# Kernel optimization log

Hardware: AMD Instinct MI355X
Metric: run time of the kernel (lower is better)

Reference implementation:

```python
import jax, jax.numpy as jnp
import numpy as np

N, L, D, H = 2, 2048, 2048, 16
HD = D // H  # head_dim = 128


def setup_inputs() -> dict:
    key = jax.random.key(0)
    k1, k2, k3, k4 = jax.random.split(key, 4)
    x = jax.random.normal(k1, (N, L, D), dtype=jnp.float32)
    pos = jax.random.normal(k2, (2, L, HD), dtype=jnp.float32)
    w_qkv = jax.random.normal(k3, (3 * D, D), dtype=jnp.float32) * (D ** -0.5)
    w_o = jax.random.normal(k4, (D, D), dtype=jnp.float32) * (D ** -0.5)
    return {"x": x, "pos": pos, "w_qkv": w_qkv, "w_o": w_o}


def rotate_half(t):
    t1, t2 = jnp.split(t, 2, axis=-1)
    return jnp.concatenate((-t2, t1), axis=-1)


def reference(x, pos, w_qkv, w_o):
    n, l, d = x.shape
    h, hd = H, HD
    qkv = jnp.einsum('nld,ed->nle', x, w_qkv)  # [N,L,3D]
    q, k, v = jnp.split(qkv, 3, axis=-1)
    q = q.reshape(n, l, h, hd)
    k = k.reshape(n, l, h, hd)
    v = v.reshape(n, l, h, hd)
    cos = pos[0][None, :, None, :]  # [1,L,1,HD]
    sin = pos[1][None, :, None, :]
    q = q * cos + rotate_half(q) * sin
    k = k * cos + rotate_half(k) * sin
    scale = hd ** -0.5
    scores = jnp.einsum('nlhd,nmhd->nhlm', q, k) * scale  # [N,H,L,L]
    causal = jnp.tril(jnp.ones((l, l), dtype=bool))
    scores = jnp.where(causal[None, None], scores, jnp.finfo(scores.dtype).min)
    attn = jax.nn.softmax(scores, axis=-1)
    o = jnp.einsum('nhlm,nmhd->nlhd', attn, v).reshape(n, l, d)
    return jnp.einsum('nld,ed->nle', o, w_o)
```

## Files before the change

### kernel.cpp

```cpp
#include <hip/hip_runtime.h>
#include <hip/hip_bf16.h>

typedef __attribute__((ext_vector_type(8))) short short8;
typedef __attribute__((ext_vector_type(4))) float f32x4;
typedef __attribute__((ext_vector_type(2))) unsigned uint2v;

#define NB 2
#define SEQ 2048
#define DM 2048
#define NHEAD 16
#define HDIM 128

__device__ __forceinline__ unsigned short f2bf(float f) {
    unsigned u = __float_as_uint(f);
    u += 0x7fffu + ((u >> 16) & 1u);
    return (unsigned short)(u >> 16);
}
__device__ __forceinline__ float bf2f(unsigned short h) {
    return __uint_as_float(((unsigned)h) << 16);
}
__device__ __forceinline__ unsigned pk2bf(float a, float b) {
    __hip_bfloat162 h = __float22bfloat162_rn(make_float2(a, b));
    return *reinterpret_cast<unsigned*>(&h);
}
__device__ __forceinline__ void gload16(const unsigned short* g, unsigned short* l) {
    __builtin_amdgcn_global_load_lds((const __attribute__((address_space(1))) void*)g,
                                     (__attribute__((address_space(3))) void*)l,
                                     16, 0, 0);
}

__global__ __launch_bounds__(256) void cvt_bf16(const float* __restrict__ a,
                                                unsigned short* __restrict__ oa, int na8,
                                                const float* __restrict__ b,
                                                unsigned short* __restrict__ ob, int nb8)
{
    const int t0 = blockIdx.x * 256 + threadIdx.x;
    const int stride = gridDim.x * 256;
    for (int i = t0; i < na8; i += stride) {
        const f32x4* src = (const f32x4*)(a + (size_t)i * 8);
        f32x4 lo = src[0], hi = src[1];
        short8 v;
#pragma unroll
        for (int j = 0; j < 4; ++j) { v[j] = (short)f2bf(lo[j]); v[j + 4] = (short)f2bf(hi[j]); }
        *(short8*)(oa + (size_t)i * 8) = v;
    }
    for (int i = t0; i < nb8; i += stride) {
        const f32x4* src = (const f32x4*)(b + (size_t)i * 8);
        f32x4 lo = src[0], hi = src[1];
        short8 v;
#pragma unroll
        for (int j = 0; j < 4; ++j) { v[j] = (short)f2bf(lo[j]); v[j + 4] = (short)f2bf(hi[j]); }
        *(short8*)(ob + (size_t)i * 8) = v;
    }
}

template<int EPI, int CPX>
__global__ __launch_bounds__(256) void gemm_m97(const unsigned short* __restrict__ A,
                                                const unsigned short* __restrict__ B,
                                                int K,
                                                unsigned short* __restrict__ qb,
                                                unsigned short* __restrict__ kb,
                                                unsigned short* __restrict__ vtb,
                                                const float* __restrict__ posp,
                                                float* __restrict__ outf)
{
    __shared__ unsigned short smem[16384];
    const int tid = threadIdx.x;
    const int lane = tid & 63, w = tid >> 6;
    const int wr = w >> 1, wc = w & 1;
    const int g = lane >> 4, fr = lane & 15;
    const int lr = lane >> 2, ls = lane & 3;
    const int x = blockIdx.x & 7, t = blockIdx.x >> 3;
    const int rp = t / (2 * CPX), wi = t % (2 * CPX);
    const int bx = x * CPX + (wi % CPX), by = rp * 2 + wi / CPX;
    const int row0 = by * 128, col0 = bx * 128;

    auto stage = [&](int b, int kt) {
        const int k0 = kt * 32;
#pragma unroll
        for (int c = 0; c < 2; ++c) {
            const int r = c * 64 + w * 16;
            gload16(A + (size_t)(row0 + r + lr) * K + k0 + ls * 8,
                    smem + b * 4096 + r * 32);
            gload16(B + (size_t)(col0 + r + lr) * K + k0 + ls * 8,
                    smem + 8192 + b * 4096 + r * 32);
        }
    };

    const f32x4 fz = {0.f, 0.f, 0.f, 0.f};
    f32x4 acc[4][4];
#pragma unroll
    for (int m = 0; m < 4; ++m)
#pragma unroll
        for (int n = 0; n < 4; ++n) acc[m][n] = fz;

    const int nk = K / 32;
    stage(0, 0);
    __syncthreads();
    for (int kt = 0; kt < nk; ++kt) {
        const int cur = kt & 1;
        if (kt + 1 < nk) stage(cur ^ 1, kt + 1);
        short8 af[4], bfv[4];
#pragma unroll
        for (int m = 0; m < 4; ++m)
            af[m] = *(const short8*)&smem[cur * 4096 + (wr * 64 + m * 16 + fr) * 32 + g * 8];
#pragma unroll
        for (int n = 0; n < 4; ++n)
            bfv[n] = *(const short8*)&smem[8192 + cur * 4096 + (wc * 64 + n * 16 + fr) * 32 + g * 8];
#pragma unroll
        for (int m = 0; m < 4; ++m)
#pragma unroll
            for (int n = 0; n < 4; ++n)
                acc[m][n] = __builtin_amdgcn_mfma_f32_16x16x32_bf16(
                    af[m], bfv[n], acc[m][n], 0, 0, 0);
        __syncthreads();
    }

    if constexpr (EPI == 0) {
#pragma unroll
        for (int m = 0; m < 4; ++m)
#pragma unroll
            for (int n = 0; n < 4; ++n)
#pragma unroll
                for (int r = 0; r < 4; ++r) {
                    int rr = row0 + wr * 64 + m * 16 + g * 4 + r;
                    int cc = col0 + wc * 64 + n * 16 + fr;
                    outf[(size_t)rr * 2048 + cc] = acc[m][n][r];
                }
    } else {
        const int which = col0 >> 11;
        const int hB = (col0 >> 7) & 15;
        const int nb_ = row0 >> 11;
        const size_t hb = (size_t)(nb_ * NHEAD + hB) * ((size_t)SEQ * HDIM);
        const int l0 = row0 & 2047;
        if (which < 2) {
#pragma unroll
            for (int m = 0; m < 4; ++m)
#pragma unroll
                for (int n = 0; n < 4; ++n)
#pragma unroll
                    for (int r = 0; r < 4; ++r) {
                        int rl = wr * 64 + m * 16 + g * 4 + r;
                        int cl = wc * 64 + n * 16 + fr;
                        smem[rl * 128 + (cl ^ ((rl & 7) * 8))] = f2bf(acc[m][n][r]);
                    }
            __syncthreads();
            unsigned short* dst = which ? kb : qb;
            const int rg = tid >> 4;
            const int s8 = (tid & 15) * 8;
            const float sgn = (s8 < 64) ? -1.f : 1.f;
#pragma unroll
            for (int j = 0; j < 8; ++j) {
                int rl = j * 16 + rg;
                int l = l0 + rl;
                int sw = (rl & 7) * 8;
                short8 own = *(const short8*)&smem[rl * 128 + (s8 ^ sw)];
                short8 par = *(const short8*)&smem[rl * 128 + ((s8 ^ 64) ^ sw)];
                const float* cp = posp + (size_t)l * HDIM + s8;
                const float* sp = cp + (size_t)SEQ * HDIM;
                f32x4 c0 = *(const f32x4*)cp, c1 = *(const f32x4*)(cp + 4);
                f32x4 s0 = *(const f32x4*)sp, s1 = *(const f32x4*)(sp + 4);
                short8 res;
#pragma unroll
                for (int e = 0; e < 8; ++e) {
                    float cc = (e < 4) ? c0[e & 3] : c1[e & 3];
                    float ss = (e < 4) ? s0[e & 3] : s1[e & 3];
                    float o = bf2f((unsigned short)own[e]);
                    float p = bf2f((unsigned short)par[e]);
                    res[e] = (short)f2bf(o * cc + sgn * p * ss);
                }
                *(short8*)(dst + hb + (size_t)l * HDIM + s8) = res;
            }
        } else {
#pragma unroll
            for (int m = 0; m < 4; ++m)
#pragma unroll
                for (int n = 0; n < 4; ++n) {
                    int lb = l0 + wr * 64 + m * 16 + g * 4;
                    int cl = wc * 64 + n * 16 + fr;
                    uint2v v;
                    v[0] = pk2bf(acc[m][n][0], acc[m][n][1]);
                    v[1] = pk2bf(acc[m][n][2], acc[m][n][3]);
                    *(uint2v*)(vtb + hb + (size_t)cl * SEQ + lb) = v;
                }
        }
    }
}

__global__ __launch_bounds__(256, 2) void attn_k(const unsigned short* __restrict__ Q,
                                                 const unsigned short* __restrict__ K,
                                                 const unsigned short* __restrict__ VT,
                                                 unsigned short* __restrict__ O)
{
    const int lb = blockIdx.x;
    const int half = lb >> 8;
    const int r0 = lb & 255;
    const int xcd = r0 & 7, idx = r0 >> 3;
    const int nh = xcd * 4 + (idx & 3);
    const int j = idx >> 2;
    const int tile = half ? j : (15 - j);
    const int tid = threadIdx.x;
    const int w = tid >> 6, lane = tid & 63;
    const int g = lane >> 4, fr = lane & 15;
    const float scale = 0.08838834764831845f;

    const unsigned short* Qh = Q + (size_t)nh * SEQ * HDIM;
    const unsigned short* Kh = K + (size_t)nh * SEQ * HDIM;
    const unsigned short* Vh = VT + (size_t)nh * SEQ * HDIM;
    const int nb = nh >> 4, h = nh & 15;

    __shared__ unsigned short Kt[2][8192];
    __shared__ unsigned short Vt[2][8192];
    __shared__ unsigned Plds[4][576];

    auto stage = [&](int bf, int kbi) {
        const int key0 = kbi * 64;
#pragma unroll
        for (int c = 0; c < 4; ++c) {
            int r = c * 16 + (tid >> 4);
            int sK = tid & 15;
            gload16(Kh + (size_t)(key0 + r) * HDIM + 8 * (sK ^ (r & 7)),
                    &Kt[bf][c * 2048 + w * 512]);
            int d = c * 32 + (tid >> 3);
            int sV = tid & 7;
            gload16(Vh + (size_t)d * SEQ + key0 + 8 * (sV ^ (d & 7)),
                    &Vt[bf][c * 2048 + w * 512]);
        }
    };

    const int qt = tile * 128 + w * 32;
    const int nkb_w = (qt + 31) >> 6;
    const int nkb_blk = 2 * tile + 1;

    short8 qf[2][4];
#pragma unroll
    for (int u = 0; u < 2; ++u)
#pragma unroll
        for (int kk = 0; kk < 4; ++kk)
            qf[u][kk] = *(const short8*)(Qh + (size_t)(qt + u * 16 + fr) * HDIM + kk * 32 + g * 8);

    const f32x4 fz = {0.f, 0.f, 0.f, 0.f};
    f32x4 oacc[2][8];
#pragma unroll
    for (int u = 0; u < 2; ++u)
#pragma unroll
        for (int f = 0; f < 8; ++f) oacc[u][f] = fz;
    float mrow[2] = {-3e38f, -3e38f}, lrow[2] = {0.f, 0.f};

    stage(0, 0);
    int buf = 0;
    __syncthreads();

    for (int kbi = 0; kbi <= nkb_blk; ++kbi) {
        if (kbi < nkb_blk) stage(buf ^ 1, kbi + 1);

        if (kbi <= nkb_w) {
            const int key0 = kbi * 64;
            f32x4 s[2][4];
#pragma unroll
            for (int u = 0; u < 2; ++u)
#pragma unroll
                for (int hh = 0; hh < 4; ++hh) s[u][hh] = fz;

            __builtin_amdgcn_s_setprio(1);
#pragma unroll
            for (int hh = 0; hh < 4; ++hh) {
                short8 kfh[4];
#pragma unroll
                for (int kk = 0; kk < 4; ++kk)
                    kfh[kk] = *(const short8*)&Kt[buf][(hh * 16 + fr) * 128 + 8 * ((4 * kk + g) ^ (fr & 7))];
#pragma unroll
                for (int u = 0; u < 2; ++u)
#pragma unroll
                    for (int kk = 0; kk < 4; ++kk)
                        s[u][hh] = __builtin_amdgcn_mfma_f32_16x16x32_bf16(kfh[kk], qf[u][kk], s[u][hh], 0, 0, 0);
            }
            __builtin_amdgcn_s_setprio(0);

#pragma unroll
            for (int u = 0; u < 2; ++u) {
                const int q = qt + u * 16 + fr;
#pragma unroll
                for (int hh = 0; hh < 4; ++hh)
#pragma unroll
                    for (int r = 0; r < 4; ++r) {
                        int key = key0 + hh * 16 + 4 * g + r;
                        float v = s[u][hh][r] * scale;
                        s[u][hh][r] = (key <= q) ? v : -1e30f;
                    }
                float mx = -3e38f;
#pragma unroll
                for (int hh = 0; hh < 4; ++hh)
                    mx = fmaxf(mx, fmaxf(fmaxf(s[u][hh][0], s[u][hh][1]),
                                         fmaxf(s[u][hh][2], s[u][hh][3])));
                mx = fmaxf(mx, __shfl_xor(mx, 16, 64));
                mx = fmaxf(mx, __shfl_xor(mx, 32, 64));
                if (!__all(mx <= mrow[u] + 8.f)) {
                    float mn = fmaxf(mrow[u], mx);
                    float al = __expf(mrow[u] - mn);
                    mrow[u] = mn;
                    lrow[u] *= al;
#pragma unroll
                    for (int f = 0; f < 8; ++f)
#pragma unroll
                        for (int r = 0; r < 4; ++r) oacc[u][f][r] *= al;
                }
                float pv[4][4];
                float ps = 0.f;
#pragma unroll
                for (int hh = 0; hh < 4; ++hh)
#pragma unroll
                    for (int r = 0; r < 4; ++r) {
                        float e = __expf(s[u][hh][r] - mrow[u]);
                        pv[hh][r] = e;
                        ps += e;
                    }
                ps += __shfl_xor(ps, 16, 64);
                ps += __shfl_xor(ps, 32, 64);
                lrow[u] += ps;
                unsigned* Pw = &Plds[w][0];
#pragma unroll
                for (int hh = 0; hh < 4; ++hh) {
                    Pw[fr * 36 + hh * 8 + 2 * g + 0] = pk2bf(pv[hh][0], pv[hh][1]);
                    Pw[fr * 36 + hh * 8 + 2 * g + 1] = pk2bf(pv[hh][2], pv[hh][3]);
                }
                asm volatile("s_waitcnt lgkmcnt(0)" ::: "memory");
                short8 pf0 = *(const short8*)&Pw[fr * 36 + g * 4];
                short8 pf1 = *(const short8*)&Pw[fr * 36 + 16 + g * 4];

                __builtin_amdgcn_s_setprio(1);
#pragma unroll
                for (int f = 0; f < 8; ++f) {
                    short8 vfa = *(const short8*)&Vt[buf][(f * 16 + fr) * 64 + 8 * (g ^ (fr & 7))];
                    short8 vfb = *(const short8*)&Vt[buf][(f * 16 + fr) * 64 + 8 * ((4 + g) ^ (fr & 7))];
                    oacc[u][f] = __builtin_amdgcn_mfma_f32_16x16x32_bf16(vfa, pf0, oacc[u][f], 0, 0, 0);
                    oacc[u][f] = __builtin_amdgcn_mfma_f32_16x16x32_bf16(vfb, pf1, oacc[u][f], 0, 0, 0);
                }
                __builtin_amdgcn_s_setprio(0);
            }
        }
        __syncthreads();
        buf ^= 1;
    }

#pragma unroll
    for (int u = 0; u < 2; ++u) {
        const float inv = 1.0f / lrow[u];
        const size_t obase = ((size_t)nb * SEQ + qt + u * 16 + fr) * DM + h * HDIM;
#pragma unroll
        for (int f = 0; f < 8; ++f) {
            uint2v v;
            v[0] = pk2bf(oacc[u][f][0] * inv, oacc[u][f][1] * inv);
            v[1] = pk2bf(oacc[u][f][2] * inv, oacc[u][f][3] * inv);
            *(uint2v*)(O + obase + f * 16 + 4 * g) = v;
        }
    }
}

extern "C" void kernel_launch(void* const* d_in, const int* in_sizes, int n_in,
                              void* d_out, int out_size, void* d_ws, size_t ws_size,
                              hipStream_t stream) {
    const float* x    = (const float*)d_in[0];
    const float* pos  = (const float*)d_in[1];
    const float* wqkv = (const float*)d_in[2];
    const float* wo   = (const float*)d_in[3];
    float* out = (float*)d_out;

    const size_t HBUF = (size_t)NB * NHEAD * SEQ * HDIM;
    unsigned short* qb   = (unsigned short*)d_ws;
    unsigned short* kbuf = qb + HBUF;
    unsigned short* vtb  = kbuf + HBUF;
    unsigned short* obx  = vtb + HBUF;
    unsigned short* wqkvbf = (unsigned short*)d_out;

    cvt_bf16<<<dim3(2048), 256, 0, stream>>>(x, obx, 1048576, wqkv, wqkvbf, 1572864);
    gemm_m97<1, 6><<<dim3(1536), 256, 0, stream>>>(obx, wqkvbf, 2048, qb, kbuf, vtb, pos, nullptr);
    attn_k<<<dim3(512), 256, 0, stream>>>(qb, kbuf, vtb, obx);
    cvt_bf16<<<dim3(512), 256, 0, stream>>>(wo, qb, 524288, wo, qb, 0);
    gemm_m97<0, 2><<<dim3(512), 256, 0, stream>>>(obx, qb, 2048, nullptr, nullptr, nullptr, nullptr, out);
}
```

Baseline: 282.1 us.

## Halve attention query tile to 64 rows and re-swizzle GEMM block order

```diff
diff --git a/kernel.cpp b/kernel.cpp
--- a/kernel.cpp
+++ b/kernel.cpp
@@ -54,7 +54,7 @@
     }
 }
 
-template<int EPI, int CPX>
+template<int EPI, int CPX, int CHALF>
 __global__ __launch_bounds__(256) void gemm_m97(const unsigned short* __restrict__ A,
                                                 const unsigned short* __restrict__ B,
                                                 int K,
@@ -70,9 +70,11 @@
     const int wr = w >> 1, wc = w & 1;
     const int g = lane >> 4, fr = lane & 15;
     const int lr = lane >> 2, ls = lane & 3;
+    constexpr int NSUB = CPX / CHALF;
     const int x = blockIdx.x & 7, t = blockIdx.x >> 3;
-    const int rp = t / (2 * CPX), wi = t % (2 * CPX);
-    const int bx = x * CPX + (wi % CPX), by = rp * 2 + wi / CPX;
+    const int ch = t / (32 * NSUB), u = t % (32 * NSUB);
+    const int rp = u / (2 * NSUB), wi = u % (2 * NSUB);
+    const int bx = x * CPX + ch * NSUB + (wi % NSUB), by = rp * 2 + wi / NSUB;
     const int row0 = by * 128, col0 = bx * 128;
 
     auto stage = [&](int b, int kt) {
@@ -193,12 +195,13 @@
                                                  unsigned short* __restrict__ O)
 {
     const int lb = blockIdx.x;
-    const int half = lb >> 8;
+    const int quart = lb >> 8;
     const int r0 = lb & 255;
     const int xcd = r0 & 7, idx = r0 >> 3;
     const int nh = xcd * 4 + (idx & 3);
     const int j = idx >> 2;
-    const int tile = half ? j : (15 - j);
+    const int tile = (quart == 0) ? (31 - j) : (quart == 1) ? j
+                   : (quart == 2) ? (23 - j) : (8 + j);
     const int tid = threadIdx.x;
     const int w = tid >> 6, lane = tid & 63;
     const int g = lane >> 4, fr = lane & 15;
@@ -228,132 +231,115 @@
         }
     };
 
-    const int qt = tile * 128 + w * 32;
-    const int nkb_w = (qt + 31) >> 6;
-    const int nkb_blk = 2 * tile + 1;
-
-    short8 qf[2][4];
-#pragma unroll
-    for (int u = 0; u < 2; ++u)
-#pragma unroll
-        for (int kk = 0; kk < 4; ++kk)
-            qf[u][kk] = *(const short8*)(Qh + (size_t)(qt + u * 16 + fr) * HDIM + kk * 32 + g * 8);
+    const int qt = tile * 64 + w * 16;
+    const int nkb = tile;
+
+    short8 qf[4];
+#pragma unroll
+    for (int kk = 0; kk < 4; ++kk)
+        qf[kk] = *(const short8*)(Qh + (size_t)(qt + fr) * HDIM + kk * 32 + g * 8);
 
     const f32x4 fz = {0.f, 0.f, 0.f, 0.f};
-    f32x4 oacc[2][8];
-#pragma unroll
-    for (int u = 0; u < 2; ++u)
-#pragma unroll
-        for (int f = 0; f < 8; ++f) oacc[u][f] = fz;
-    float mrow[2] = {-3e38f, -3e38f}, lrow[2] = {0.f, 0.f};
+    f32x4 oacc[8];
+#pragma unroll
+    for (int f = 0; f < 8; ++f) oacc[f] = fz;
+    float mrow = -3e38f, lrow = 0.f;
 
     stage(0, 0);
     int buf = 0;
     __syncthreads();
 
-    for (int kbi = 0; kbi <= nkb_blk; ++kbi) {
-        if (kbi < nkb_blk) stage(buf ^ 1, kbi + 1);
-
-        if (kbi <= nkb_w) {
-            const int key0 = kbi * 64;
-            f32x4 s[2][4];
-#pragma unroll
-            for (int u = 0; u < 2; ++u)
-#pragma unroll
-                for (int hh = 0; hh < 4; ++hh) s[u][hh] = fz;
-
-            __builtin_amdgcn_s_setprio(1);
-#pragma unroll
-            for (int hh = 0; hh < 4; ++hh) {
-                short8 kfh[4];
-#pragma unroll
-                for (int kk = 0; kk < 4; ++kk)
-                    kfh[kk] = *(const short8*)&Kt[buf][(hh * 16 + fr) * 128 + 8 * ((4 * kk + g) ^ (fr & 7))];
-#pragma unroll
-                for (int u = 0; u < 2; ++u)
-#pragma unroll
-                    for (int kk = 0; kk < 4; ++kk)
-                        s[u][hh] = __builtin_amdgcn_mfma_f32_16x16x32_bf16(kfh[kk], qf[u][kk], s[u][hh], 0, 0, 0);
+    for (int kbi = 0; kbi <= nkb; ++kbi) {
+        if (kbi < nkb) stage(buf ^ 1, kbi + 1);
+
+        const int key0 = kbi * 64;
+        f32x4 s[4];
+#pragma unroll
+        for (int hh = 0; hh < 4; ++hh) s[hh] = fz;
+
+        __builtin_amdgcn_s_setprio(1);
+#pragma unroll
+        for (int hh = 0; hh < 4; ++hh) {
+            short8 kfh[4];
+#pragma unroll
+            for (int kk = 0; kk < 4; ++kk)
+                kfh[kk] = *(const short8*)&Kt[buf][(hh * 16 + fr) * 128 + 8 * ((4 * kk + g) ^ (fr & 7))];
+#pragma unroll
+            for (int kk = 0; kk < 4; ++kk)
+                s[hh] = __builtin_amdgcn_mfma_f32_16x16x32_bf16(kfh[kk], qf[kk], s[hh], 0, 0, 0);
+        }
+        __builtin_amdgcn_s_setprio(0);
+
+        const int q = qt + fr;
+#pragma unroll
+        for (int hh = 0; hh < 4; ++hh)
+#pragma unroll
+            for (int r = 0; r < 4; ++r) {
+                int key = key0 + hh * 16 + 4 * g + r;
+                float v = s[hh][r] * scale;
+                s[hh][r] = (key <= q) ? v : -1e30f;
             }
-            __builtin_amdgcn_s_setprio(0);
-
-#pragma unroll
-            for (int u = 0; u < 2; ++u) {
-                const int q = qt + u * 16 + fr;
-#pragma unroll
-                for (int hh = 0; hh < 4; ++hh)
-#pragma unroll
-                    for (int r = 0; r < 4; ++r) {
-                        int key = key0 + hh * 16 + 4 * g + r;
-                        float v = s[u][hh][r] * scale;
-                        s[u][hh][r] = (key <= q) ? v : -1e30f;
-                    }
-                float mx = -3e38f;
-#pragma unroll
-                for (int hh = 0; hh < 4; ++hh)
-                    mx = fmaxf(mx, fmaxf(fmaxf(s[u][hh][0], s[u][hh][1]),
-                                         fmaxf(s[u][hh][2], s[u][hh][3])));
-                mx = fmaxf(mx, __shfl_xor(mx, 16, 64));
-                mx = fmaxf(mx, __shfl_xor(mx, 32, 64));
-                if (!__all(mx <= mrow[u] + 8.f)) {
-                    float mn = fmaxf(mrow[u], mx);
-                    float al = __expf(mrow[u] - mn);
-                    mrow[u] = mn;
-                    lrow[u] *= al;
-#pragma unroll
-                    for (int f = 0; f < 8; ++f)
-#pragma unroll
-                        for (int r = 0; r < 4; ++r) oacc[u][f][r] *= al;
-                }
-                float pv[4][4];
-                float ps = 0.f;
-#pragma unroll
-                for (int hh = 0; hh < 4; ++hh)
-#pragma unroll
-                    for (int r = 0; r < 4; ++r) {
-                        float e = __expf(s[u][hh][r] - mrow[u]);
-                        pv[hh][r] = e;
-                        ps += e;
-                    }
-                ps += __shfl_xor(ps, 16, 64);
-                ps += __shfl_xor(ps, 32, 64);
-                lrow[u] += ps;
-                unsigned* Pw = &Plds[w][0];
-#pragma unroll
-                for (int hh = 0; hh < 4; ++hh) {
-                    Pw[fr * 36 + hh * 8 + 2 * g + 0] = pk2bf(pv[hh][0], pv[hh][1]);
-                    Pw[fr * 36 + hh * 8 + 2 * g + 1] = pk2bf(pv[hh][2], pv[hh][3]);
-                }
-                asm volatile("s_waitcnt lgkmcnt(0)" ::: "memory");
-                short8 pf0 = *(const short8*)&Pw[fr * 36 + g * 4];
-                short8 pf1 = *(const short8*)&Pw[fr * 36 + 16 + g * 4];
-
-                __builtin_amdgcn_s_setprio(1);
-#pragma unroll
-                for (int f = 0; f < 8; ++f) {
-                    short8 vfa = *(const short8*)&Vt[buf][(f * 16 + fr) * 64 + 8 * (g ^ (fr & 7))];
-                    short8 vfb = *(const short8*)&Vt[buf][(f * 16 + fr) * 64 + 8 * ((4 + g) ^ (fr & 7))];
-                    oacc[u][f] = __builtin_amdgcn_mfma_f32_16x16x32_bf16(vfa, pf0, oacc[u][f], 0, 0, 0);
-                    oacc[u][f] = __builtin_amdgcn_mfma_f32_16x16x32_bf16(vfb, pf1, oacc[u][f], 0, 0, 0);
-                }
-                __builtin_amdgcn_s_setprio(0);
+        float mx = -3e38f;
+#pragma unroll
+        for (int hh = 0; hh < 4; ++hh)
+            mx = fmaxf(mx, fmaxf(fmaxf(s[hh][0], s[hh][1]), fmaxf(s[hh][2], s[hh][3])));
+        mx = fmaxf(mx, __shfl_xor(mx, 16, 64));
+        mx = fmaxf(mx, __shfl_xor(mx, 32, 64));
+        if (!__all(mx <= mrow + 8.f)) {
+            float mn = fmaxf(mrow, mx);
+            float al = __expf(mrow - mn);
+            mrow = mn;
+            lrow *= al;
+#pragma unroll
+            for (int f = 0; f < 8; ++f)
+#pragma unroll
+                for (int r = 0; r < 4; ++r) oacc[f][r] *= al;
+        }
+        float pv[4][4];
+        float ps = 0.f;
+#pragma unroll
+        for (int hh = 0; hh < 4; ++hh)
+#pragma unroll
+            for (int r = 0; r < 4; ++r) {
+                float e = __expf(s[hh][r] - mrow);
+                pv[hh][r] = e;
+                ps += e;
             }
-        }
+        ps += __shfl_xor(ps, 16, 64);
+        ps += __shfl_xor(ps, 32, 64);
+        lrow += ps;
+        unsigned* Pw = &Plds[w][0];
+#pragma unroll
+        for (int hh = 0; hh < 4; ++hh) {
+            Pw[fr * 36 + hh * 8 + 2 * g + 0] = pk2bf(pv[hh][0], pv[hh][1]);
+            Pw[fr * 36 + hh * 8 + 2 * g + 1] = pk2bf(pv[hh][2], pv[hh][3]);
+        }
+        asm volatile("s_waitcnt lgkmcnt(0)" ::: "memory");
+        short8 pf0 = *(const short8*)&Pw[fr * 36 + g * 4];
+        short8 pf1 = *(const short8*)&Pw[fr * 36 + 16 + g * 4];
+
+        __builtin_amdgcn_s_setprio(1);
+#pragma unroll
+        for (int f = 0; f < 8; ++f) {
+            short8 vfa = *(const short8*)&Vt[buf][(f * 16 + fr) * 64 + 8 * (g ^ (fr & 7))];
+            short8 vfb = *(const short8*)&Vt[buf][(f * 16 + fr) * 64 + 8 * ((4 + g) ^ (fr & 7))];
+            oacc[f] = __builtin_amdgcn_mfma_f32_16x16x32_bf16(vfa, pf0, oacc[f], 0, 0, 0);
+            oacc[f] = __builtin_amdgcn_mfma_f32_16x16x32_bf16(vfb, pf1, oacc[f], 0, 0, 0);
+        }
+        __builtin_amdgcn_s_setprio(0);
+
         __syncthreads();
         buf ^= 1;
     }
 
-#pragma unroll
-    for (int u = 0; u < 2; ++u) {
-        const float inv = 1.0f / lrow[u];
-        const size_t obase = ((size_t)nb * SEQ + qt + u * 16 + fr) * DM + h * HDIM;
-#pragma unroll
-        for (int f = 0; f < 8; ++f) {
-            uint2v v;
-            v[0] = pk2bf(oacc[u][f][0] * inv, oacc[u][f][1] * inv);
-            v[1] = pk2bf(oacc[u][f][2] * inv, oacc[u][f][3] * inv);
-            *(uint2v*)(O + obase + f * 16 + 4 * g) = v;
-        }
+    const float inv = 1.0f / lrow;
+    const size_t obase = ((size_t)nb * SEQ + qt + fr) * DM + h * HDIM;
+#pragma unroll
+    for (int f = 0; f < 8; ++f) {
+        uint2v v;
+        v[0] = pk2bf(oacc[f][0] * inv, oacc[f][1] * inv);
+        v[1] = pk2bf(oacc[f][2] * inv, oacc[f][3] * inv);
+        *(uint2v*)(O + obase + f * 16 + 4 * g) = v;
     }
 }
 
@@ -374,8 +360,8 @@
     unsigned short* wqkvbf = (unsigned short*)d_out;
 
     cvt_bf16<<<dim3(2048), 256, 0, stream>>>(x, obx, 1048576, wqkv, wqkvbf, 1572864);
-    gemm_m97<1, 6><<<dim3(1536), 256, 0, stream>>>(obx, wqkvbf, 2048, qb, kbuf, vtb, pos, nullptr);
-    attn_k<<<dim3(512), 256, 0, stream>>>(qb, kbuf, vtb, obx);
+    gemm_m97<1, 6, 2><<<dim3(1536), 256, 0, stream>>>(obx, wqkvbf, 2048, qb, kbuf, vtb, pos, nullptr);
+    attn_k<<<dim3(1024), 256, 0, stream>>>(qb, kbuf, vtb, obx);
     cvt_bf16<<<dim3(512), 256, 0, stream>>>(wo, qb, 524288, wo, qb, 0);
-    gemm_m97<0, 2><<<dim3(512), 256, 0, stream>>>(obx, qb, 2048, nullptr, nullptr, nullptr, nullptr, out);
-}
+    gemm_m97<0, 2, 1><<<dim3(512), 256, 0, stream>>>(obx, qb, 2048, nullptr, nullptr, nullptr, nullptr, out);
+}
```

Result: no change. 280.9 us (-0.4%).
